# Kernel optimization log

Measured on AMD Instinct MI355X. Metric: run time of the kernel, lower is better.

The kernel has to match this reference:

```python
import jax, jax.numpy as jnp
import numpy as np

GAMMA = 0.96875
SCALE_BASE = 512.0


def _fixed_pos_embedding(scale):
    # scale: (L, d) where d = head_dim // 2
    L, d = scale.shape
    inv_freq = 1.0 / (10000.0 ** (jnp.arange(d, dtype=jnp.float32) / d))
    sinusoid = jnp.arange(L, dtype=jnp.float32)[:, None] * inv_freq  # (L, d)
    return jnp.sin(sinusoid), jnp.cos(sinusoid)


def _rotate_every_two(x):
    # (..., D) -> (..., D) with pairs (x0, x1) -> (-x1, x0)
    x1 = x[..., ::2]
    x2 = x[..., 1::2]
    return jnp.stack((-x2, x1), axis=-1).reshape(x.shape)


def _dup_interleave(m):
    # (L, d) -> (L, 2d), each column duplicated (matches rotary pairing)
    return jnp.repeat(m, 2, axis=-1)


def xpos(x, offset=0, downscale=False):
    # x: (B, S, D). Standard torchscale-style XPos rotary embedding.
    S, D = x.shape[-2], x.shape[-1]
    scale_vec = (jnp.arange(0, D, 2, dtype=jnp.float32) + 0.4 * D) / (1.4 * D)  # (D/2,)
    min_pos = -(S + offset) // 2
    max_pos = S + offset + min_pos
    power = jnp.arange(min_pos, max_pos, dtype=jnp.float32) / SCALE_BASE  # (S+offset,)
    scale = scale_vec ** power[:, None]  # (S+offset, D/2)
    sin, cos = _fixed_pos_embedding(scale)
    if scale.shape[0] > S:  # keep the last S positions
        scale, sin, cos = scale[-S:], sin[-S:], cos[-S:]
    if downscale:
        scale = 1.0 / scale
    sin = _dup_interleave(sin * scale)  # (S, D)
    cos = _dup_interleave(cos * scale)  # (S, D)
    return x * cos + _rotate_every_two(x) * sin


def _decay_mask(S, dtype):
    # D[n, m] = gamma^(n-m) if n >= m else 0  (lower triangular)
    m = jnp.arange(S)
    diff = m[:, None] - m  # (S, S)
    causal = diff >= 0
    exp = jnp.where(causal, diff, 0).astype(dtype)
    return jnp.where(causal, jnp.asarray(GAMMA, dtype) ** exp, jnp.zeros((), dtype))


def setup_inputs() -> dict:
    key = jax.random.key(0)
    kx, kq, kk, kv = jax.random.split(key, 4)
    B, S, H, Dh = 4, 4096, 2048, 256
    return {
        "x": jax.random.normal(kx, (B, S, H), dtype=jnp.float32),
        "w_q": jax.random.normal(kq, (H, Dh), dtype=jnp.float32),
        "w_k": jax.random.normal(kk, (H, Dh), dtype=jnp.float32),
        "w_v": jax.random.normal(kv, (H, Dh), dtype=jnp.float32),
    }


def reference(x, w_q, w_k, w_v):
    # x: (B, S, H) -> out: (B, S, Dh)
    B, S, _ = x.shape
    decay = _decay_mask(S, x.dtype)[None]  # (1, S, S)
    q = xpos(x @ w_q)                       # (B, S, Dh)
    k = xpos(x @ w_k, downscale=True)       # (B, S, Dh)
    v = x @ w_v                             # (B, S, Dh)
    ret = jnp.einsum("bsd,btd->bst", q, k) * decay  # (B, S, S)
    return jnp.einsum("bst,btd->bsd", ret, v)       # (B, S, Dh)
```

## Files before the change

kernel.cpp:

```cpp
#include <hip/hip_runtime.h>
#include <cstddef>
#include <cstdint>

#define Bn 4
#define Sn 4096
#define Hn 2048
#define Dn 256

typedef float f32x16 __attribute__((ext_vector_type(16)));
typedef short bf16x8 __attribute__((ext_vector_type(8)));

#define AS3 __attribute__((address_space(3)))
#define AS1 __attribute__((address_space(1)))

#define L2G -0.045803689613125f
#define GC 2.9526131e-4f

__device__ __forceinline__ unsigned short f2bf(float f) {
  union { float f; unsigned int u; } a; a.f = f;
  unsigned int r = a.u + 0x7fffu + ((a.u >> 16) & 1u);
  return (unsigned short)(r >> 16);
}
__device__ __forceinline__ float bf2f(unsigned int b) {
  union { unsigned int u; float f; } a; a.u = b << 16;
  return a.f;
}

__global__ __launch_bounds__(256) void xbf_kernel(const float* __restrict__ x,
                                                  unsigned short* __restrict__ xb) {
  const size_t g = (size_t)blockIdx.x * 256 + threadIdx.x;
  const float* src = x + g * 16;
  unsigned short* dst = xb + g * 16;
  uint4 o0, o1;
  {
    float4 v0 = ((const float4*)src)[0];
    float4 v1 = ((const float4*)src)[1];
    float4 v2 = ((const float4*)src)[2];
    float4 v3 = ((const float4*)src)[3];
    o0.x = f2bf(v0.x) | ((unsigned int)f2bf(v0.y) << 16);
    o0.y = f2bf(v0.z) | ((unsigned int)f2bf(v0.w) << 16);
    o0.z = f2bf(v1.x) | ((unsigned int)f2bf(v1.y) << 16);
    o0.w = f2bf(v1.z) | ((unsigned int)f2bf(v1.w) << 16);
    o1.x = f2bf(v2.x) | ((unsigned int)f2bf(v2.y) << 16);
    o1.y = f2bf(v2.z) | ((unsigned int)f2bf(v2.w) << 16);
    o1.z = f2bf(v3.x) | ((unsigned int)f2bf(v3.y) << 16);
    o1.w = f2bf(v3.z) | ((unsigned int)f2bf(v3.w) << 16);
  }
  ((uint4*)dst)[0] = o0;
  ((uint4*)dst)[1] = o1;
}

__global__ __launch_bounds__(256) void wt_build(const float* __restrict__ wq,
                                                const float* __restrict__ wk,
                                                const float* __restrict__ wv,
                                                unsigned short* __restrict__ wt) {
  __shared__ __align__(16) unsigned short T[64][72];
  const int tid = threadIdx.x;
  const int k0 = blockIdx.x * 64;
  const int n0 = blockIdx.y * 64;
  const float* w = (n0 < 256) ? wq : (n0 < 512 ? wk : wv);
  const int nc0 = n0 & 255;
#pragma unroll
  for (int it = 0; it < 2; ++it) {
    int flat = it * 256 + tid;
    int r = flat >> 3, c8 = flat & 7;
    const float* src = w + (size_t)(k0 + r) * 256 + nc0 + c8 * 8;
    float4 v0 = *(const float4*)src;
    float4 v1 = *(const float4*)(src + 4);
    T[c8 * 8 + 0][r] = f2bf(v0.x); T[c8 * 8 + 1][r] = f2bf(v0.y);
    T[c8 * 8 + 2][r] = f2bf(v0.z); T[c8 * 8 + 3][r] = f2bf(v0.w);
    T[c8 * 8 + 4][r] = f2bf(v1.x); T[c8 * 8 + 5][r] = f2bf(v1.y);
    T[c8 * 8 + 6][r] = f2bf(v1.z); T[c8 * 8 + 7][r] = f2bf(v1.w);
  }
  __syncthreads();
#pragma unroll
  for (int it = 0; it < 2; ++it) {
    int flat = it * 256 + tid;
    int nr = flat >> 3, kc8 = flat & 7;
    int n = n0 + nr;
    int kc_sw = kc8 ^ (n & 7);
    uint4 val = *(const uint4*)&T[nr][kc8 * 8];
    *(uint4*)((char*)wt + (size_t)n * 4096 + (size_t)k0 * 2 + kc_sw * 16) = val;
  }
}

__global__ __launch_bounds__(256, 3) void proj2_kernel(const unsigned short* __restrict__ xb,
                                                       const unsigned short* __restrict__ wt,
                                                       unsigned short* __restrict__ qkv) {
  __shared__ __align__(16) unsigned short As[128 * 64];
  __shared__ __align__(16) unsigned short Bs[128 * 64];
  const int tid = threadIdx.x;
  const int lane = tid & 63;
  const int wid = tid >> 6;
  const int wr = wid >> 1, wc = wid & 1;
  const int m0 = blockIdx.x * 128;
  const int n0 = blockIdx.y * 128;
  const int l31 = lane & 31, lh = lane >> 5;

  f32x16 acc[2][2];
#pragma unroll
  for (int i = 0; i < 2; ++i)
#pragma unroll
    for (int j = 0; j < 2; ++j) acc[i][j] = 0.0f;

  for (int k0 = 0; k0 < Hn; k0 += 64) {
    AS3 char* ldsa = (AS3 char*)As;
    AS3 char* ldsb = (AS3 char*)Bs;
#pragma unroll
    for (int i = 0; i < 4; ++i) {
      int ou = i * 4096 + wid * 1024;
      int o = ou + lane * 16;
      int row = o >> 7, colB = o & 127;
      const char* srcA = (const char*)xb + (size_t)(m0 + row) * 4096 + k0 * 2 + (colB ^ ((row & 7) << 4));
      __builtin_amdgcn_global_load_lds((const AS1 unsigned int*)srcA,
                                       (AS3 unsigned int*)(ldsa + ou), 16, 0, 0);
      const char* srcB = (const char*)wt + (size_t)(n0 + row) * 4096 + k0 * 2 + colB;
      __builtin_amdgcn_global_load_lds((const AS1 unsigned int*)srcB,
                                       (AS3 unsigned int*)(ldsb + ou), 16, 0, 0);
    }
    __syncthreads();
#pragma unroll
    for (int kc = 0; kc < 4; ++kc) {
      const int kb = kc * 32 + lh * 16;
      bf16x8 a[2], b[2];
#pragma unroll
      for (int i = 0; i < 2; ++i) {
        int mr = wr * 64 + i * 32 + l31;
        a[i] = *(const bf16x8*)((const char*)As + mr * 128 + (kb ^ ((mr & 7) << 4)));
        int nr = wc * 64 + i * 32 + l31;
        b[i] = *(const bf16x8*)((const char*)Bs + nr * 128 + (kb ^ ((nr & 7) << 4)));
      }
#pragma unroll
      for (int i = 0; i < 2; ++i)
#pragma unroll
        for (int j = 0; j < 2; ++j)
          acc[i][j] = __builtin_amdgcn_mfma_f32_32x32x16_bf16(a[i], b[j], acc[i][j], 0, 0, 0);
    }
    __syncthreads();
  }
  const bool khalf = (n0 >= 256 && n0 < 512);
#pragma unroll
  for (int i = 0; i < 2; ++i)
#pragma unroll
    for (int j = 0; j < 2; ++j)
#pragma unroll
      for (int reg = 0; reg < 16; ++reg) {
        int m = m0 + wr * 64 + i * 32 + (reg & 3) + 8 * (reg >> 2) + 4 * lh;
        int n = n0 + wc * 64 + j * 32 + l31;
        if (khalf) n = 256 + ((n - 256) ^ ((m & 7) << 3));
        qkv[(size_t)m * 768 + n] = f2bf(acc[i][j][reg]);
      }
}

__global__ __launch_bounds__(256, 2) void proj_kernel(const float* __restrict__ x,
                                                      const unsigned short* __restrict__ wt,
                                                      unsigned short* __restrict__ qkv) {
  __shared__ __align__(16) unsigned short As[128 * 64];
  __shared__ __align__(16) unsigned short Bs[128 * 64];
  const int tid = threadIdx.x;
  const int lane = tid & 63;
  const int wid = tid >> 6;
  const int wr = wid >> 1, wc = wid & 1;
  const int m0 = blockIdx.x * 128;
  const int n0 = blockIdx.y * 128;
  const int l31 = lane & 31, lh = lane >> 5;

  f32x16 acc[2][2];
#pragma unroll
  for (int i = 0; i < 2; ++i)
#pragma unroll
    for (int j = 0; j < 2; ++j) acc[i][j] = 0.0f;

  for (int k0 = 0; k0 < Hn; k0 += 64) {
    {
      AS3 char* ldsb = (AS3 char*)Bs;
#pragma unroll
      for (int i = 0; i < 4; ++i) {
        int ou = i * 4096 + wid * 1024;
        int o = ou + lane * 16;
        int row = o >> 7, col = o & 127;
        const char* src = (const char*)wt + (size_t)(n0 + row) * 4096 + k0 * 2 + col;
        __builtin_amdgcn_global_load_lds((const AS1 unsigned int*)src,
                                         (AS3 unsigned int*)(ldsb + ou), 16, 0, 0);
      }
    }
#pragma unroll
    for (int i = 0; i < 4; ++i) {
      int o = i * 256 + tid;
      int row = o >> 3, c8 = o & 7;
      const float* src = x + (size_t)(m0 + row) * 2048 + k0 + c8 * 8;
      float4 v0 = *(const float4*)src;
      float4 v1 = *(const float4*)(src + 4);
      uint4 val;
      val.x = f2bf(v0.x) | ((unsigned int)f2bf(v0.y) << 16);
      val.y = f2bf(v0.z) | ((unsigned int)f2bf(v0.w) << 16);
      val.z = f2bf(v1.x) | ((unsigned int)f2bf(v1.y) << 16);
      val.w = f2bf(v1.z) | ((unsigned int)f2bf(v1.w) << 16);
      *(uint4*)((char*)As + row * 128 + ((c8 * 16) ^ ((row & 7) << 4))) = val;
    }
    __syncthreads();
#pragma unroll
    for (int kc = 0; kc < 4; ++kc) {
      const int kb = kc * 32 + lh * 16;
      bf16x8 a[2], b[2];
#pragma unroll
      for (int i = 0; i < 2; ++i) {
        int mr = wr * 64 + i * 32 + l31;
        a[i] = *(const bf16x8*)((const char*)As + mr * 128 + (kb ^ ((mr & 7) << 4)));
        int nr = wc * 64 + i * 32 + l31;
        b[i] = *(const bf16x8*)((const char*)Bs + nr * 128 + (kb ^ ((nr & 7) << 4)));
      }
#pragma unroll
      for (int i = 0; i < 2; ++i)
#pragma unroll
        for (int j = 0; j < 2; ++j)
          acc[i][j] = __builtin_amdgcn_mfma_f32_32x32x16_bf16(a[i], b[j], acc[i][j], 0, 0, 0);
    }
    __syncthreads();
  }
  const bool khalf = (n0 >= 256 && n0 < 512);
#pragma unroll
  for (int i = 0; i < 2; ++i)
#pragma unroll
    for (int j = 0; j < 2; ++j)
#pragma unroll
      for (int reg = 0; reg < 16; ++reg) {
        int m = m0 + wr * 64 + i * 32 + (reg & 3) + 8 * (reg >> 2) + 4 * lh;
        int n = n0 + wc * 64 + j * 32 + l31;
        if (khalf) n = 256 + ((n - 256) ^ ((m & 7) << 3));
        qkv[(size_t)m * 768 + n] = f2bf(acc[i][j][reg]);
      }
}

__global__ __launch_bounds__(256) void xpos_kernel(unsigned short* __restrict__ qkv) {
  const int g = blockIdx.x * 256 + threadIdx.x;
  const int m = g >> 5;
  const int c = g & 31;
  const float s = (float)(m & (Sn - 1));
  unsigned short* qrow = qkv + (size_t)m * 768;
  const int csw = c ^ (m & 7);
  uint4 qv = *(uint4*)(qrow + c * 8);
  uint4 kv = *(uint4*)(qrow + 256 + csw * 8);
  unsigned int* qu = (unsigned int*)&qv;
  unsigned int* ku = (unsigned int*)&kv;
  const float pw = (s - 2048.0f) * (1.0f / 512.0f);
  const float gp = exp2f((float)(m & 255) * L2G);
#pragma unroll
  for (int p = 0; p < 4; ++p) {
    const int jp = c * 4 + p;
    const float invf = exp2f((float)jp * (-13.287712379549449f / 128.0f));
    float sn, cs;
    sincosf(s * invf, &sn, &cs);
    const float sv = (2.0f * jp + 102.4f) * (1.0f / 358.4f);
    const float scq = exp2f(pw * log2f(sv)) * gp;
    const float sci = 1.0f / scq;
    float q0 = bf2f(qu[p] & 0xffffu), q1 = bf2f(qu[p] >> 16);
    float k0 = bf2f(ku[p] & 0xffffu), k1 = bf2f(ku[p] >> 16);
    float q0r = (q0 * cs - q1 * sn) * scq;
    float q1r = (q1 * cs + q0 * sn) * scq;
    float k0r = (k0 * cs - k1 * sn) * sci;
    float k1r = (k1 * cs + k0 * sn) * sci;
    qu[p] = f2bf(q0r) | ((unsigned int)f2bf(q1r) << 16);
    ku[p] = f2bf(k0r) | ((unsigned int)f2bf(k1r) << 16);
  }
  *(uint4*)(qrow + c * 8) = qv;
  *(uint4*)(qrow + 256 + csw * 8) = kv;
}

__global__ __launch_bounds__(256) void kvt_build(const unsigned short* __restrict__ qkv,
                                                 unsigned short* __restrict__ kt,
                                                 unsigned short* __restrict__ vt) {
  __shared__ __align__(16) unsigned short Tk[64][72];
  __shared__ __align__(16) unsigned short Tv[64][72];
  const int tid = threadIdx.x;
  const int t0 = blockIdx.x * 64;
  const int d0 = blockIdx.y * 64;
  const int b = blockIdx.z;
  const size_t rowb = ((size_t)b * Sn + t0) * 1536;
#pragma unroll
  for (int it = 0; it < 2; ++it) {
    int flat = it * 256 + tid;
    int r = flat >> 3, c8 = flat & 7;
    int kc = (d0 >> 3) + c8;
    int kcs = kc ^ (r & 7);
    uint4 kvv = *(const uint4*)((const char*)qkv + rowb + (size_t)r * 1536 + 512 + kcs * 16);
    uint4 vvv = *(const uint4*)((const char*)qkv + rowb + (size_t)r * 1536 + 1024 + (size_t)(d0 + c8 * 8) * 2);
    const unsigned short* ke = (const unsigned short*)&kvv;
    const unsigned short* ve = (const unsigned short*)&vvv;
#pragma unroll
    for (int e = 0; e < 8; ++e) { Tk[c8 * 8 + e][r] = ke[e]; Tv[c8 * 8 + e][r] = ve[e]; }
  }
  __syncthreads();
#pragma unroll
  for (int it = 0; it < 2; ++it) {
    int flat = it * 256 + tid;
    int dr = flat >> 3, tc8 = flat & 7;
    *(uint4*)(kt + (size_t)(b * 256 + d0 + dr) * 4096 + t0 + tc8 * 8) = *(const uint4*)&Tk[dr][tc8 * 8];
    *(uint4*)(vt + (size_t)(b * 256 + d0 + dr) * 4096 + t0 + tc8 * 8) = *(const uint4*)&Tv[dr][tc8 * 8];
  }
}

__global__ __launch_bounds__(256) void mbuild_kernel(const unsigned short* __restrict__ kt,
                                                     const unsigned short* __restrict__ vt,
                                                     unsigned short* __restrict__ mt) {
  const int tid = threadIdx.x;
  const int lane = tid & 63;
  const int wid = tid >> 6;
  const int l31 = lane & 31, lh = lane >> 5;
  const int jc = blockIdx.x;
  const int quad = blockIdx.y;
  const int b = blockIdx.z;
  const int d2w = ((quad >> 1) * 2 + (wid >> 1)) * 64;
  const int d1w = ((quad & 1) * 2 + (wid & 1)) * 64;
  const size_t tb = (size_t)jc * 256;

  f32x16 acc[2][2];
#pragma unroll
  for (int i = 0; i < 2; ++i)
#pragma unroll
    for (int j = 0; j < 2; ++j) acc[i][j] = 0.0f;

#pragma unroll 2
  for (int dc = 0; dc < 16; ++dc) {
    const int ko = dc * 32 + lh * 16;
    bf16x8 a[2], bb[2];
#pragma unroll
    for (int i = 0; i < 2; ++i) {
      a[i]  = *(const bf16x8*)((const char*)vt + ((size_t)(b * 256 + d2w + i * 32 + l31) * 4096 + tb) * 2 + ko);
      bb[i] = *(const bf16x8*)((const char*)kt + ((size_t)(b * 256 + d1w + i * 32 + l31) * 4096 + tb) * 2 + ko);
    }
#pragma unroll
    for (int i = 0; i < 2; ++i)
#pragma unroll
      for (int j = 0; j < 2; ++j)
        acc[i][j] = __builtin_amdgcn_mfma_f32_32x32x16_bf16(a[i], bb[j], acc[i][j], 0, 0, 0);
  }
  unsigned short* dst = mt + ((size_t)(b * 16 + jc) << 16);
#pragma unroll
  for (int i = 0; i < 2; ++i)
#pragma unroll
    for (int j = 0; j < 2; ++j)
#pragma unroll
      for (int reg = 0; reg < 16; ++reg) {
        int row = d2w + i * 32 + (reg & 3) + 8 * (reg >> 2) + 4 * lh;
        int col = d1w + j * 32 + l31;
        dst[row * 256 + col] = f2bf(acc[i][j][reg]);
      }
}

__global__ __launch_bounds__(256) void scan_kernel(unsigned short* __restrict__ mt) {
  const int e0 = (blockIdx.x * 256 + threadIdx.x) * 4;
  const int b = blockIdx.y;
  unsigned short* base = mt + ((size_t)b << 20);
  float s0 = 0.f, s1 = 0.f, s2 = 0.f, s3 = 0.f;
  for (int j = 1; j < 16; ++j) {
    unsigned short* p = base + ((size_t)(j - 1) << 16) + e0;
    uint2 mv = *(const uint2*)p;
    s0 = GC * (s0 + bf2f(mv.x & 0xffffu));
    s1 = GC * (s1 + bf2f(mv.x >> 16));
    s2 = GC * (s2 + bf2f(mv.y & 0xffffu));
    s3 = GC * (s3 + bf2f(mv.y >> 16));
    uint2 w;
    w.x = f2bf(s0) | ((unsigned int)f2bf(s1) << 16);
    w.y = f2bf(s2) | ((unsigned int)f2bf(s3) << 16);
    *(uint2*)p = w;
  }
}

__global__ __launch_bounds__(256, 2) void retc_kernel(const unsigned short* __restrict__ qkv,
                                                      const unsigned short* __restrict__ vt,
                                                      const unsigned short* __restrict__ mt,
                                                      float* __restrict__ out) {
  __shared__ float cmb[2][32][128];
  const int tid = threadIdx.x;
  const int lane = tid & 63;
  const int tw = tid >> 6;
  const int l31 = lane & 31, lh = lane >> 5;
  const int st = blockIdx.x;
  const int dh = blockIdx.y;
  const int b = blockIdx.z;
  const int j = st >> 3;
  const int base = st & ~7;
  const int s0 = st * 32;
  const int d0 = dh * 128;

  bf16x8 qf[16];
  {
    const char* qrow = (const char*)qkv + ((size_t)b * Sn + s0 + l31) * 1536;
#pragma unroll
    for (int dc = 0; dc < 16; ++dc)
      qf[dc] = *(const bf16x8*)(qrow + dc * 32 + lh * 16);
  }

  f32x16 acc[4];
#pragma unroll
  for (int i = 0; i < 4; ++i) acc[i] = 0.0f;

  if (j > 0) {
    const char* Sj = (const char*)mt + ((size_t)(b * 16 + j - 1) << 17);
#pragma unroll
    for (int dcl = 0; dcl < 4; ++dcl) {
      const int dc = tw * 4 + dcl;
#pragma unroll
      for (int g = 0; g < 4; ++g) {
        const int d2 = d0 + g * 32 + l31;
        bf16x8 sbf = *(const bf16x8*)(Sj + (size_t)d2 * 512 + dc * 32 + lh * 16);
        acc[g] = __builtin_amdgcn_mfma_f32_32x32x16_bf16(qf[dc], sbf, acc[g], 0, 0, 0);
      }
    }
  }

  const int sg = s0 + l31;
  const int ksw = (l31 & 7) << 4;
  for (int tt = base; tt <= st; ++tt) {
    if (((tt - base) & 3) != tw) continue;
    const bool msk = (tt == st);
    const int t0 = tt * 32;

    f32x16 sacc = 0.0f;
    const char* krow = (const char*)qkv + ((size_t)b * Sn + t0 + l31) * 1536 + 512;
    __builtin_amdgcn_s_setprio(1);
#pragma unroll
    for (int dc = 0; dc < 16; ++dc) {
      bf16x8 kf = *(const bf16x8*)(krow + ((dc * 32 + lh * 16) ^ ksw));
      sacc = __builtin_amdgcn_mfma_f32_32x32x16_bf16(kf, qf[dc], sacc, 0, 0, 0);
    }
    __builtin_amdgcn_s_setprio(0);

    unsigned int P[8];
#pragma unroll
    for (int k = 0; k < 8; ++k) {
      const int r0 = 2 * k;
      float f0 = sacc[r0], f1 = sacc[r0 + 1];
      if (msk) {
        const int tg0 = t0 + (r0 & 3) + 8 * (r0 >> 2) + 4 * lh;
        f0 = (sg - tg0 >= 0) ? f0 : 0.0f;
        f1 = (sg - tg0 - 1 >= 0) ? f1 : 0.0f;
      }
      unsigned int pk;
      asm("v_cvt_pk_bf16_f32 %0, %1, %2" : "=v"(pk) : "v"(f0), "v"(f1));
      P[k] = pk;
    }
    asm volatile("v_permlane32_swap_b32 %0, %1" : "+v"(P[0]), "+v"(P[2]));
    asm volatile("v_permlane32_swap_b32 %0, %1" : "+v"(P[1]), "+v"(P[3]));
    asm volatile("v_permlane32_swap_b32 %0, %1" : "+v"(P[4]), "+v"(P[6]));
    asm volatile("v_permlane32_swap_b32 %0, %1" : "+v"(P[5]), "+v"(P[7]));

    __builtin_amdgcn_s_setprio(1);
#pragma unroll
    for (int kc = 0; kc < 2; ++kc) {
      uint4 pw;
      pw.x = P[kc * 4 + 0]; pw.y = P[kc * 4 + 1];
      pw.z = P[kc * 4 + 2]; pw.w = P[kc * 4 + 3];
      bf16x8 pf = *(const bf16x8*)&pw;
#pragma unroll
      for (int g = 0; g < 4; ++g) {
        const int d = d0 + g * 32 + l31;
        bf16x8 vf = *(const bf16x8*)((const char*)vt +
            ((size_t)(b * 256 + d) * 4096 + t0) * 2 + kc * 32 + lh * 16);
        acc[g] = __builtin_amdgcn_mfma_f32_32x32x16_bf16(pf, vf, acc[g], 0, 0, 0);
      }
    }
    __builtin_amdgcn_s_setprio(0);
  }

  if (tw >= 2) {
#pragma unroll
    for (int g = 0; g < 4; ++g)
#pragma unroll
      for (int reg = 0; reg < 16; ++reg) {
        int sl = (reg & 3) + 8 * (reg >> 2) + 4 * lh;
        cmb[tw - 2][sl][g * 32 + l31] = acc[g][reg];
      }
  }
  __syncthreads();
  if (tw < 2) {
#pragma unroll
    for (int g = 0; g < 4; ++g)
#pragma unroll
      for (int reg = 0; reg < 16; ++reg) {
        int sl = (reg & 3) + 8 * (reg >> 2) + 4 * lh;
        acc[g][reg] += cmb[tw][sl][g * 32 + l31];
      }
  }
  __syncthreads();
  if (tw == 1) {
#pragma unroll
    for (int g = 0; g < 4; ++g)
#pragma unroll
      for (int reg = 0; reg < 16; ++reg) {
        int sl = (reg & 3) + 8 * (reg >> 2) + 4 * lh;
        cmb[0][sl][g * 32 + l31] = acc[g][reg];
      }
  }
  __syncthreads();
  if (tw == 0) {
#pragma unroll
    for (int g = 0; g < 4; ++g)
#pragma unroll
      for (int reg = 0; reg < 16; ++reg) {
        int sl = (reg & 3) + 8 * (reg >> 2) + 4 * lh;
        int c = g * 32 + l31;
        out[((size_t)(b * Sn + s0 + sl)) * 256 + d0 + c] = acc[g][reg] + cmb[0][sl][c];
      }
  }
}

extern "C" void kernel_launch(void* const* d_in, const int* in_sizes, int n_in,
                              void* d_out, int out_size, void* d_ws, size_t ws_size,
                              hipStream_t stream) {
  (void)in_sizes; (void)n_in; (void)out_size;
  const float* x  = (const float*)d_in[0];
  const float* wq = (const float*)d_in[1];
  const float* wk = (const float*)d_in[2];
  const float* wv = (const float*)d_in[3];
  float* out = (float*)d_out;
  char* ws = (char*)d_ws;

  unsigned short* qkv = (unsigned short*)(ws);
  unsigned short* vt  = (unsigned short*)(ws + 25165824);
  unsigned short* kt  = (unsigned short*)(ws + 33554432);
  unsigned short* mt  = (unsigned short*)(ws + 41943040);

  const size_t NEED_BIG = 95420416;
  if (ws_size >= NEED_BIG) {
    unsigned short* xb = (unsigned short*)(ws + 25165824);
    unsigned short* wt = (unsigned short*)(ws + 92274688);
    xbf_kernel<<<8192, 256, 0, stream>>>(x, xb);
    wt_build<<<dim3(32, 12), 256, 0, stream>>>(wq, wk, wv, wt);
    proj2_kernel<<<dim3(128, 6), 256, 0, stream>>>(xb, wt, qkv);
  } else {
    unsigned short* wt = (unsigned short*)(ws + 41943040);
    wt_build<<<dim3(32, 12), 256, 0, stream>>>(wq, wk, wv, wt);
    proj_kernel<<<dim3(128, 6), 256, 0, stream>>>(x, wt, qkv);
  }
  xpos_kernel<<<2048, 256, 0, stream>>>(qkv);
  kvt_build<<<dim3(64, 4, 4), 256, 0, stream>>>(qkv, kt, vt);
  mbuild_kernel<<<dim3(16, 4, 4), 256, 0, stream>>>(kt, vt, mt);
  scan_kernel<<<dim3(64, 4), 256, 0, stream>>>(mt);
  retc_kernel<<<dim3(128, 2, 4), 256, 0, stream>>>(qkv, vt, mt, out);
}
```

Baseline: 186.0 us.

## Fuse xpos rotary scaling and K/V transpose into projection GEMM epilogue

The bf16 projection kernel now applies the XPos rotation and decay scaling to Q and K in registers, using lane shuffles to fetch each pair partner. It also writes transposed K and V directly through an LDS staging tile. This removes the separate xpos_kernel and kvt_build launches and their extra round trips through global memory on the big-workspace path. In exchange the epilogue gets heavier (sincos, exp2 and an LDS transpose), and the workspace requirement grows because xb and wt are moved to higher offsets.

```diff
diff --git a/kernel.cpp b/kernel.cpp
--- a/kernel.cpp
+++ b/kernel.cpp
@@ -84,11 +84,14 @@
   }
 }
 
-__global__ __launch_bounds__(256, 3) void proj2_kernel(const unsigned short* __restrict__ xb,
-                                                       const unsigned short* __restrict__ wt,
-                                                       unsigned short* __restrict__ qkv) {
-  __shared__ __align__(16) unsigned short As[128 * 64];
-  __shared__ __align__(16) unsigned short Bs[128 * 64];
+__global__ __launch_bounds__(256, 3) void proj2f_kernel(const unsigned short* __restrict__ xb,
+                                                        const unsigned short* __restrict__ wt,
+                                                        unsigned short* __restrict__ qkv,
+                                                        unsigned short* __restrict__ kt,
+                                                        unsigned short* __restrict__ vt) {
+  __shared__ __align__(16) char smem[32768];
+  unsigned short* As = (unsigned short*)smem;
+  unsigned short* Bs = (unsigned short*)(smem + 16384);
   const int tid = threadIdx.x;
   const int lane = tid & 63;
   const int wid = tid >> 6;
@@ -138,18 +141,92 @@
     }
     __syncthreads();
   }
-  const bool khalf = (n0 >= 256 && n0 < 512);
-#pragma unroll
-  for (int i = 0; i < 2; ++i)
-#pragma unroll
-    for (int j = 0; j < 2; ++j)
+
+  const int kind = n0 >> 8;
+  const int n0q = n0 & 255;
+  const int bidx = m0 >> 12;
+  const int t0b = m0 & 4095;
+
+  if (kind < 2) {
+    float invf[2], l2sv[2];
+#pragma unroll
+    for (int j = 0; j < 2; ++j) {
+      const int jp = (n0q + wc * 64 + j * 32 + l31) >> 1;
+      invf[j] = exp2f((float)jp * (-13.287712379549449f / 128.0f));
+      l2sv[j] = log2f((2.0f * jp + 102.4f) * (1.0f / 358.4f));
+    }
+    const int odd = l31 & 1;
+#pragma unroll
+    for (int i = 0; i < 2; ++i)
 #pragma unroll
       for (int reg = 0; reg < 16; ++reg) {
-        int m = m0 + wr * 64 + i * 32 + (reg & 3) + 8 * (reg >> 2) + 4 * lh;
-        int n = n0 + wc * 64 + j * 32 + l31;
-        if (khalf) n = 256 + ((n - 256) ^ ((m & 7) << 3));
-        qkv[(size_t)m * 768 + n] = f2bf(acc[i][j][reg]);
-      }
+        const int mm = m0 + wr * 64 + i * 32 + (reg & 3) + 8 * (reg >> 2) + 4 * lh;
+        const float s = (float)(mm & (Sn - 1));
+        const float pw = (s - 2048.0f) * (1.0f / 512.0f);
+        const float tl = (float)(mm & 255) * L2G;
+#pragma unroll
+        for (int j = 0; j < 2; ++j) {
+          float v = acc[i][j][reg];
+          float p = __shfl_xor(v, 1, 64);
+          float sn, cs;
+          sincosf(s * invf[j], &sn, &cs);
+          float ex = pw * l2sv[j] + tl;
+          float e = exp2f(kind == 0 ? ex : -ex);
+          float r = odd ? (v * cs + p * sn) : (v * cs - p * sn);
+          acc[i][j][reg] = r * e;
+        }
+      }
+  }
+
+  if (kind == 0) {
+#pragma unroll
+    for (int i = 0; i < 2; ++i)
+#pragma unroll
+      for (int j = 0; j < 2; ++j)
+#pragma unroll
+        for (int reg = 0; reg < 16; ++reg) {
+          int m = m0 + wr * 64 + i * 32 + (reg & 3) + 8 * (reg >> 2) + 4 * lh;
+          int n = n0q + wc * 64 + j * 32 + l31;
+          qkv[(size_t)m * 768 + n] = f2bf(acc[i][j][reg]);
+        }
+  } else {
+    if (kind == 1) {
+#pragma unroll
+      for (int i = 0; i < 2; ++i)
+#pragma unroll
+        for (int j = 0; j < 2; ++j)
+#pragma unroll
+          for (int reg = 0; reg < 16; ++reg) {
+            int m = m0 + wr * 64 + i * 32 + (reg & 3) + 8 * (reg >> 2) + 4 * lh;
+            int d = n0q + wc * 64 + j * 32 + l31;
+            qkv[(size_t)m * 768 + 256 + (d ^ ((m & 7) << 3))] = f2bf(acc[i][j][reg]);
+          }
+    }
+#pragma unroll
+    for (int i = 0; i < 2; ++i)
+#pragma unroll
+      for (int j = 0; j < 2; ++j) {
+        const int dl = wc * 64 + j * 32 + l31;
+#pragma unroll
+        for (int k8 = 0; k8 < 8; ++k8) {
+          const int r0 = 2 * k8;
+          const int t = wr * 64 + i * 32 + (r0 & 3) + 8 * (r0 >> 2) + 4 * lh;
+          unsigned int pk;
+          asm("v_cvt_pk_bf16_f32 %0, %1, %2" : "=v"(pk)
+              : "v"(acc[i][j][r0]), "v"(acc[i][j][r0 + 1]));
+          *(unsigned int*)(smem + dl * 256 + ((2 * t) ^ ((dl & 7) << 4))) = pk;
+        }
+      }
+    __syncthreads();
+    unsigned short* dst = (kind == 1) ? kt : vt;
+#pragma unroll
+    for (int p = 0; p < 8; ++p) {
+      const int fl = p * 256 + tid;
+      const int dl = fl >> 4, t8 = fl & 15;
+      uint4 val = *(const uint4*)(smem + dl * 256 + ((t8 * 16) ^ ((dl & 7) << 4)));
+      *(uint4*)(dst + (size_t)(bidx * 256 + n0q + dl) * 4096 + t0b + t8 * 8) = val;
+    }
+  }
 }
 
 __global__ __launch_bounds__(256, 2) void proj_kernel(const float* __restrict__ x,
@@ -522,20 +599,20 @@
   unsigned short* kt  = (unsigned short*)(ws + 33554432);
   unsigned short* mt  = (unsigned short*)(ws + 41943040);
 
-  const size_t NEED_BIG = 95420416;
+  const size_t NEED_BIG = 120586240;
   if (ws_size >= NEED_BIG) {
-    unsigned short* xb = (unsigned short*)(ws + 25165824);
-    unsigned short* wt = (unsigned short*)(ws + 92274688);
+    unsigned short* xb = (unsigned short*)(ws + 50331648);
+    unsigned short* wt = (unsigned short*)(ws + 117440512);
     xbf_kernel<<<8192, 256, 0, stream>>>(x, xb);
     wt_build<<<dim3(32, 12), 256, 0, stream>>>(wq, wk, wv, wt);
-    proj2_kernel<<<dim3(128, 6), 256, 0, stream>>>(xb, wt, qkv);
+    proj2f_kernel<<<dim3(128, 6), 256, 0, stream>>>(xb, wt, qkv, kt, vt);
   } else {
     unsigned short* wt = (unsigned short*)(ws + 41943040);
     wt_build<<<dim3(32, 12), 256, 0, stream>>>(wq, wk, wv, wt);
     proj_kernel<<<dim3(128, 6), 256, 0, stream>>>(x, wt, qkv);
-  }
-  xpos_kernel<<<2048, 256, 0, stream>>>(qkv);
-  kvt_build<<<dim3(64, 4, 4), 256, 0, stream>>>(qkv, kt, vt);
+    xpos_kernel<<<2048, 256, 0, stream>>>(qkv);
+    kvt_build<<<dim3(64, 4, 4), 256, 0, stream>>>(qkv, kt, vt);
+  }
   mbuild_kernel<<<dim3(16, 4, 4), 256, 0, stream>>>(kt, vt, mt);
   scan_kernel<<<dim3(64, 4), 256, 0, stream>>>(mt);
   retc_kernel<<<dim3(128, 2, 4), 256, 0, stream>>>(qkv, vt, mt, out);
```

Result: slower. 636.2 us (+242.1%).
